# Kernel optimization log

Measured on AMD Instinct MI355X. Metric: run time of the kernel, lower is better.

## Reference

```python
import jax, jax.numpy as jnp
import numpy as np
from jax import lax

NUM_STEPS = 32
NUM_CLASSES = 10
HIDDEN = 1024


def setup_inputs() -> dict:
    key = jax.random.key(0)
    ks = jax.random.split(key, 4)
    B, H, W, C = 8, 1024, 2048, 4
    x = jax.random.normal(ks[0], (B, H, W, C), dtype=jnp.float32)
    conv_w = jax.random.normal(ks[1], (C,), dtype=jnp.float32) * 0.5
    conv_b = jnp.zeros((1,), dtype=jnp.float32)
    w1 = jax.random.normal(ks[2], (HIDDEN, W), dtype=jnp.float32) * (1.0 / np.sqrt(W))
    b1 = jnp.zeros((HIDDEN,), dtype=jnp.float32)
    w2 = jax.random.normal(ks[3], (NUM_CLASSES, HIDDEN), dtype=jnp.float32) * (1.0 / np.sqrt(HIDDEN))
    b2 = jnp.zeros((NUM_CLASSES,), dtype=jnp.float32)
    beta1 = jnp.full((1,), 0.95, dtype=jnp.float32)
    thr1 = jnp.ones((1,), dtype=jnp.float32)
    beta2 = jnp.full((1,), 0.95, dtype=jnp.float32)
    thr2 = jnp.ones((1,), dtype=jnp.float32)
    return {"x": x, "conv_w": conv_w, "conv_b": conv_b, "w1": w1, "b1": b1,
            "beta1": beta1, "thr1": thr1, "w2": w2, "b2": b2,
            "beta2": beta2, "thr2": thr2}


def _leaky_scan(inp_t, beta, thr):
    # inp_t: [T, ...]; snntorch Leaky, reset_mechanism='subtract', reset_delay=False
    b = jnp.clip(beta, 0.0, 1.0)

    def step(mem, u):
        mem = b * mem + u
        spk = (mem > thr).astype(u.dtype)   # heaviside spike
        mem = mem - spk * thr               # subtract reset (no delay)
        return mem, spk

    mem0 = jnp.zeros(inp_t.shape[1:], dtype=inp_t.dtype)
    _, spks = lax.scan(step, mem0, inp_t)
    return spks  # [T, ...]


def reference(x, conv_w, conv_b, w1, b1, beta1, thr1, w2, b2, beta2, thr2):
    # x: [B, H, W, 4]; 1x1 conv over 4 antenna channels -> 1 channel
    xf = jnp.einsum('bhwc,c->bhw', x, conv_w) + conv_b[0]       # [B, H, W]
    B, H, W = xf.shape
    G = H // NUM_STEPS
    xr = xf.reshape(B, G, NUM_STEPS, W)                          # [B, G, T, 2048]
    h = jnp.einsum('bgtw,dw->bgtd', xr, w1) + b1                 # [B, G, T, D]
    spks1 = _leaky_scan(jnp.moveaxis(h, 2, 0), beta1, thr1)      # [T, B, G, D]
    s = spks1.sum(axis=0)                                        # [B, G, D]
    h2 = jnp.einsum('bgd,cd->bgc', s, w2) + b2                   # [B, G, C]
    spks2 = _leaky_scan(jnp.moveaxis(h2, 1, 0), beta2, thr2)     # [G, B, C]
    logits = spks2.sum(axis=0)                                   # [B, C]
    return jax.nn.softmax(logits, axis=1)
```

## Files before the change

kernel.cpp:

```cpp
#include <hip/hip_runtime.h>

#define TSTEPS 32
#define HID 1024
#define NCLS 10
#define BATCH 8
#define GGRP 32
#define MROWS 8192
#define GK 2048
#define GN 1024
#define BUFSH 24576
#define CLDS 40

typedef __attribute__((ext_vector_type(8))) short bf16x8;
typedef __attribute__((ext_vector_type(16))) float f32x16;

__device__ __forceinline__ unsigned short bf16_rne(float v) {
    unsigned u = __builtin_bit_cast(unsigned, v);
    return (unsigned short)((u + 0x7FFFu + ((u >> 16) & 1u)) >> 16);
}
__device__ __forceinline__ float bf16_f(unsigned short h) {
    unsigned u = (unsigned)h << 16;
    return __builtin_bit_cast(float, u);
}
__device__ __forceinline__ void gload16(const unsigned short* g, unsigned short* l) {
    __builtin_amdgcn_global_load_lds(
        (const __attribute__((address_space(1))) void*)g,
        (__attribute__((address_space(3))) void*)l, 16, 0, 0);
}


__global__ __launch_bounds__(256) void conv_pack_kernel(
    const float4* __restrict__ x, const float* __restrict__ cw,
    const float* __restrict__ cb,
    unsigned short* __restrict__ Ahi, unsigned short* __restrict__ Alo)
{
    __shared__ __align__(16) unsigned short lh[128 * CLDS];
    __shared__ __align__(16) unsigned short ll[128 * CLDS];
    const int rb = blockIdx.x >> 6;
    const int kb = blockIdx.x & 63;
    const float c0 = cw[0], c1 = cw[1], c2 = cw[2], c3 = cw[3], cbv = cb[0];
    const int tid = threadIdx.x;

#pragma unroll
    for (int p = 0; p < 16; ++p) {
        int i = p * 256 + tid;
        int row = i >> 5, px = i & 31;
        float4 a = x[(size_t)(rb * 128 + row) * 2048 + kb * 32 + px];
        float v = a.x * c0 + a.y * c1 + a.z * c2 + a.w * c3 + cbv;
        unsigned short h = bf16_rne(v);
        lh[row * CLDS + px] = h;
        ll[row * CLDS + px] = bf16_rne(v - bf16_f(h));
    }
    __syncthreads();

#pragma unroll
    for (int cc = 0; cc < 2; ++cc) {
        int c = tid + cc * 256;
        int u = c >> 6, w = c & 63;
        int row = (u >> 1) * 32 + (w & 31);
        int ko  = (u & 1) * 2 + (w >> 5);
        bf16x8 h8 = *(const bf16x8*)(lh + row * CLDS + ko * 8);
        bf16x8 l8 = *(const bf16x8*)(ll + row * CLDS + ko * 8);
        size_t off = ((size_t)blockIdx.x * 512 + c) * 8;
        *(bf16x8*)(Ahi + off) = h8;
        *(bf16x8*)(Alo + off) = l8;
    }
}

__global__ __launch_bounds__(256) void wpack_kernel(
    const float* __restrict__ wsrc, unsigned short* __restrict__ Bhi,
    unsigned short* __restrict__ Blo)
{
    const int kb  = blockIdx.x & 63;
    const int cbk = blockIdx.x >> 6;
    const int tid = threadIdx.x;
#pragma unroll
    for (int cc = 0; cc < 4; ++cc) {
        int c = tid + cc * 256;
        int u = c >> 6, w = c & 63;
        int col = cbk * 256 + (u >> 1) * 32 + (w & 31);
        int k0  = kb * 32 + (u & 1) * 16 + (w >> 5) * 8;
        const float* pw = wsrc + ((size_t)col * 2048 + k0);
        bf16x8 h8, l8;
#pragma unroll
        for (int e = 0; e < 8; ++e) {
            float v = pw[e];
            unsigned short h = bf16_rne(v);
            h8[e] = (short)h;
            l8[e] = (short)bf16_rne(v - bf16_f(h));
        }
        size_t off = ((size_t)blockIdx.x * 1024 + c) * 8;
        *(bf16x8*)(Bhi + off) = h8;
        *(bf16x8*)(Blo + off) = l8;
    }
}

__global__ __launch_bounds__(512) void gemm_scan_kernel(
    const unsigned short* __restrict__ Ahi, const unsigned short* __restrict__ Alo,
    const unsigned short* __restrict__ Bhi, const unsigned short* __restrict__ Blo,
    const float* __restrict__ bias,
    const float* __restrict__ beta1, const float* __restrict__ thr1,
    float* __restrict__ S)
{
    __shared__ __align__(16) unsigned short sm[3 * BUFSH];

    const int tid = threadIdx.x;
    const int lane = tid & 63, wv = tid >> 6;
    const int wr = wv >> 2, wc = wv & 3;
    const int by = blockIdx.x & 63;
    const int bx = blockIdx.x >> 6;

    const unsigned short* gAh = Ahi + (size_t)by * 262144;
    const unsigned short* gAl = Alo + (size_t)by * 262144;
    const unsigned short* gBh = Bhi + (size_t)bx * 524288;
    const unsigned short* gBl = Blo + (size_t)bx * 524288;

    f32x16 acc[2][2];
#pragma unroll
    for (int i = 0; i < 2; ++i)
#pragma unroll
        for (int j = 0; j < 2; ++j) acc[i][j] = (f32x16)0.f;

    bf16x8 fr[2][16];

#define STAGE(buf, kb_)                                                          \
    {                                                                            \
        unsigned short* dst = sm + (buf) * BUFSH;                                \
        const size_t ao = (size_t)(kb_) * 4096 + tid * 8;                        \
        const size_t bo = (size_t)(kb_) * 8192 + tid * 8;                        \
        gload16(gAh + ao, dst + tid * 8);                                        \
        gload16(gAl + ao, dst + 4096 + tid * 8);                                 \
        gload16(gBh + bo, dst + 8192 + tid * 8);                                 \
        gload16(gBh + bo + 4096, dst + 12288 + tid * 8);                         \
        gload16(gBl + bo, dst + 16384 + tid * 8);                                \
        gload16(gBl + bo + 4096, dst + 20480 + tid * 8);                         \
    }

#define READF(s, bufp)                                                           \
    {                                                                            \
        const unsigned short* bp_ = (bufp);                                      \
        _Pragma("unroll")                                                        \
        for (int i = 0; i < 2; ++i)                                              \
            _Pragma("unroll")                                                    \
            for (int kh = 0; kh < 2; ++kh) {                                     \
                int ua = (((wr * 2 + i) * 2 + kh) << 9) + fo;                    \
                fr[s][(i * 2 + kh) * 2 + 0] = *(const bf16x8*)(bp_ + ua);        \
                fr[s][(i * 2 + kh) * 2 + 1] = *(const bf16x8*)(bp_ + 4096 + ua); \
            }                                                                    \
        _Pragma("unroll")                                                        \
        for (int j = 0; j < 2; ++j)                                              \
            _Pragma("unroll")                                                    \
            for (int kh = 0; kh < 2; ++kh) {                                     \
                int ub = (((wc * 2 + j) * 2 + kh) << 9) + fo;                    \
                fr[s][8 + (j * 2 + kh) * 2 + 0] = *(const bf16x8*)(bp_ + 8192 + ub);  \
                fr[s][8 + (j * 2 + kh) * 2 + 1] = *(const bf16x8*)(bp_ + 16384 + ub); \
            }                                                                    \
    }

#define MFMAF(s)                                                                 \
    {                                                                            \
        _Pragma("unroll")                                                        \
        for (int kh = 0; kh < 2; ++kh) {                                         \
            _Pragma("unroll")                                                    \
            for (int i = 0; i < 2; ++i)                                          \
                _Pragma("unroll")                                                \
                for (int j = 0; j < 2; ++j)                                      \
                    acc[i][j] = __builtin_amdgcn_mfma_f32_32x32x16_bf16(         \
                        fr[s][(i * 2 + kh) * 2], fr[s][8 + (j * 2 + kh) * 2],    \
                        acc[i][j], 0, 0, 0);                                     \
            _Pragma("unroll")                                                    \
            for (int i = 0; i < 2; ++i)                                          \
                _Pragma("unroll")                                                \
                for (int j = 0; j < 2; ++j)                                      \
                    acc[i][j] = __builtin_amdgcn_mfma_f32_32x32x16_bf16(         \
                        fr[s][(i * 2 + kh) * 2], fr[s][8 + (j * 2 + kh) * 2 + 1],\
                        acc[i][j], 0, 0, 0);                                     \
            _Pragma("unroll")                                                    \
            for (int i = 0; i < 2; ++i)                                          \
                _Pragma("unroll")                                                \
                for (int j = 0; j < 2; ++j)                                      \
                    acc[i][j] = __builtin_amdgcn_mfma_f32_32x32x16_bf16(         \
                        fr[s][(i * 2 + kh) * 2 + 1], fr[s][8 + (j * 2 + kh) * 2],\
                        acc[i][j], 0, 0, 0);                                     \
        }                                                                        \
    }

#define KSTEP(SC, SN, KB)                                                        \
    {                                                                            \
        if ((KB) < 63) asm volatile("s_waitcnt vmcnt(6)" ::: "memory");          \
        else           asm volatile("s_waitcnt vmcnt(0)" ::: "memory");          \
        asm volatile("s_waitcnt lgkmcnt(0)" ::: "memory");                       \
        __builtin_amdgcn_sched_barrier(0);                                       \
        __builtin_amdgcn_s_barrier();                                            \
        if ((KB) <= 61) STAGE(((KB) + 2) % 3, (KB) + 2);                         \
        READF(SN, sm + ((KB) % 3) * BUFSH);                                      \
        MFMAF(SC);                                                               \
    }

    STAGE(0, 0);
    STAGE(1, 1);
    STAGE(2, 2);
    asm volatile("s_waitcnt vmcnt(12)" ::: "memory");
    __builtin_amdgcn_s_barrier();
    const int fo = ((lane & 31) + 32 * (lane >> 5)) * 8;
    READF(0, sm);

    for (int kb = 1; kb < 63; kb += 2) {
        KSTEP(0, 1, kb);
        KSTEP(1, 0, kb + 1);
    }
    KSTEP(0, 1, 63);
    asm volatile("s_waitcnt lgkmcnt(0)" ::: "memory");
    __builtin_amdgcn_sched_barrier(0);
    MFMAF(1);
    __syncthreads();

    float* sb = (float*)sm;
    const float bclamp = fminf(fmaxf(beta1[0], 0.f), 1.f);
    const float th = thr1[0];
    const int sbg = tid >> 8;
    const int scol = tid & 255;
    const float bv = bias[bx * 256 + scol];

#pragma unroll
    for (int band = 0; band < 2; ++band) {
        if (wr == band) {
#pragma unroll
            for (int i = 0; i < 2; ++i)
#pragma unroll
                for (int j = 0; j < 2; ++j)
#pragma unroll
                    for (int r = 0; r < 16; ++r) {
                        int lr = i * 32 + (r & 3) + 8 * (r >> 2) + 4 * (lane >> 5);
                        int lc = wc * 64 + j * 32 + (lane & 31);
                        sb[lr * 256 + lc] = acc[i][j][r];
                    }
        }
        __syncthreads();
        float mem = 0.f, cnt = 0.f;
#pragma unroll
        for (int t = 0; t < TSTEPS; ++t) {
            float u = sb[(sbg * 32 + t) * 256 + scol] + bv;
            mem = bclamp * mem + u;
            float spk = mem > th ? 1.f : 0.f;
            mem -= spk * th;
            cnt += spk;
        }
        int bgg = by * 4 + band * 2 + sbg;
        S[(size_t)bgg * GN + bx * 256 + scol] = cnt;
        __syncthreads();
    }
}

__global__ __launch_bounds__(256) void fc2_kernel(
    const float* __restrict__ s, const float* __restrict__ w2,
    const float* __restrict__ b2, float* __restrict__ h2)
{
    int bg  = blockIdx.x;
    int tid = threadIdx.x;
    const float* sp = s + (size_t)bg * HID;
    float part[NCLS];
#pragma unroll
    for (int c = 0; c < NCLS; ++c) part[c] = 0.f;
    for (int d = tid; d < HID; d += 256) {
        float sv = sp[d];
#pragma unroll
        for (int c = 0; c < NCLS; ++c) part[c] += sv * w2[c * HID + d];
    }
#pragma unroll
    for (int c = 0; c < NCLS; ++c)
        for (int off = 32; off > 0; off >>= 1)
            part[c] += __shfl_down(part[c], off, 64);
    __shared__ float red[NCLS][4];
    int wave = tid >> 6, lanei = tid & 63;
    if (lanei == 0)
#pragma unroll
        for (int c = 0; c < NCLS; ++c) red[c][wave] = part[c];
    __syncthreads();
    if (tid < NCLS) {
        float v = red[tid][0] + red[tid][1] + red[tid][2] + red[tid][3] + b2[tid];
        h2[bg * NCLS + tid] = v;
    }
}

__global__ __launch_bounds__(128) void scan2_kernel(
    const float* __restrict__ h2, const float* __restrict__ beta2,
    const float* __restrict__ thr2, float* __restrict__ out)
{
    __shared__ float logits[BATCH][NCLS];
    int t = threadIdx.x;
    if (t < BATCH * NCLS) {
        int b = t / NCLS, c = t % NCLS;
        float bb = fminf(fmaxf(beta2[0], 0.f), 1.f);
        float th = thr2[0];
        float mem = 0.f, lg = 0.f;
        for (int g = 0; g < GGRP; ++g) {
            float u = h2[(b * GGRP + g) * NCLS + c];
            mem = bb * mem + u;
            float spk = mem > th ? 1.f : 0.f;
            mem -= spk * th;
            lg += spk;
        }
        logits[b][c] = lg;
    }
    __syncthreads();
    if (t < BATCH) {
        float mx = -1e30f;
        for (int c = 0; c < NCLS; ++c) mx = fmaxf(mx, logits[t][c]);
        float e[NCLS];
        float sum = 0.f;
        for (int c = 0; c < NCLS; ++c) { e[c] = expf(logits[t][c] - mx); sum += e[c]; }
        for (int c = 0; c < NCLS; ++c) out[t * NCLS + c] = e[c] / sum;
    }
}

extern "C" void kernel_launch(void* const* d_in, const int* in_sizes, int n_in,
                              void* d_out, int out_size, void* d_ws, size_t ws_size,
                              hipStream_t stream)
{
    const float* x     = (const float*)d_in[0];
    const float* cw    = (const float*)d_in[1];
    const float* cb    = (const float*)d_in[2];
    const float* w1    = (const float*)d_in[3];
    const float* b1    = (const float*)d_in[4];
    const float* beta1 = (const float*)d_in[5];
    const float* thr1  = (const float*)d_in[6];
    const float* w2    = (const float*)d_in[7];
    const float* b2    = (const float*)d_in[8];
    const float* beta2 = (const float*)d_in[9];
    const float* thr2  = (const float*)d_in[10];
    float* out = (float*)d_out;

    unsigned short* ahi = (unsigned short*)d_ws;
    unsigned short* alo = ahi + (size_t)MROWS * GK;
    unsigned short* bhi = alo + (size_t)MROWS * GK;
    unsigned short* blo = bhi + (size_t)GN * GK;
    float* s  = (float*)(blo + (size_t)GN * GK);
    float* h2 = s + (size_t)BATCH * GGRP * HID;

    conv_pack_kernel<<<4096, 256, 0, stream>>>((const float4*)x, cw, cb, ahi, alo);
    wpack_kernel    <<<256, 256, 0, stream>>>(w1, bhi, blo);
    gemm_scan_kernel<<<256, 512, 0, stream>>>(ahi, alo, bhi, blo, b1, beta1, thr1, s);
    fc2_kernel      <<<256, 256, 0, stream>>>(s, w2, b2, h2);
    scan2_kernel    <<<1, 128, 0, stream>>>(h2, beta2, thr2, out);
}
```

Before: 154.9 us.

## Split GEMM tiles to 128x128 with 256-thread blocks and double buffering

Halves the GEMM N-tile from 256 to 128 columns, so the grid doubles to 512 blocks of 256 threads (4 waves in a 2x2 layout). The B packing and the wpack grid change to match. The LDS pipeline drops from triple to double buffering, and each step now waits on vmcnt(0). The intent is better CU occupancy (two blocks per CU, 512 blocks over 256 CUs), at the cost of less load/compute overlap and twice the A-tile traffic. The spike scan epilogue is simplified to a single LDS pass.

```diff
diff --git a/kernel.cpp b/kernel.cpp
--- a/kernel.cpp
+++ b/kernel.cpp
@@ -8,7 +8,7 @@
 #define MROWS 8192
 #define GK 2048
 #define GN 1024
-#define BUFSH 24576
+#define BUFSH 16384
 #define CLDS 40
 
 typedef __attribute__((ext_vector_type(8))) short bf16x8;
@@ -75,12 +75,12 @@
     const int cbk = blockIdx.x >> 6;
     const int tid = threadIdx.x;
 #pragma unroll
-    for (int cc = 0; cc < 4; ++cc) {
+    for (int cc = 0; cc < 2; ++cc) {
         int c = tid + cc * 256;
         int u = c >> 6, w = c & 63;
-        int col = cbk * 256 + (u >> 1) * 32 + (w & 31);
-        int k0  = kb * 32 + (u & 1) * 16 + (w >> 5) * 8;
-        const float* pw = wsrc + ((size_t)col * 2048 + k0);
+        int row = (u >> 1) * 32 + (w & 31);
+        int k0  = (u & 1) * 16 + (w >> 5) * 8;
+        const float* pw = wsrc + ((size_t)(cbk * 128 + row) * 2048 + kb * 32 + k0);
         bf16x8 h8, l8;
 #pragma unroll
         for (int e = 0; e < 8; ++e) {
@@ -89,31 +89,31 @@
             h8[e] = (short)h;
             l8[e] = (short)bf16_rne(v - bf16_f(h));
         }
-        size_t off = ((size_t)blockIdx.x * 1024 + c) * 8;
+        size_t off = ((size_t)blockIdx.x * 512 + c) * 8;
         *(bf16x8*)(Bhi + off) = h8;
         *(bf16x8*)(Blo + off) = l8;
     }
 }
 
-__global__ __launch_bounds__(512) void gemm_scan_kernel(
+__global__ __launch_bounds__(256, 2) void gemm_scan_kernel(
     const unsigned short* __restrict__ Ahi, const unsigned short* __restrict__ Alo,
     const unsigned short* __restrict__ Bhi, const unsigned short* __restrict__ Blo,
     const float* __restrict__ bias,
     const float* __restrict__ beta1, const float* __restrict__ thr1,
     float* __restrict__ S)
 {
-    __shared__ __align__(16) unsigned short sm[3 * BUFSH];
+    __shared__ __align__(16) unsigned short sm[2 * BUFSH];
 
     const int tid = threadIdx.x;
     const int lane = tid & 63, wv = tid >> 6;
-    const int wr = wv >> 2, wc = wv & 3;
+    const int wr = wv >> 1, wc = wv & 1;
     const int by = blockIdx.x & 63;
     const int bx = blockIdx.x >> 6;
 
     const unsigned short* gAh = Ahi + (size_t)by * 262144;
     const unsigned short* gAl = Alo + (size_t)by * 262144;
-    const unsigned short* gBh = Bhi + (size_t)bx * 524288;
-    const unsigned short* gBl = Blo + (size_t)bx * 524288;
+    const unsigned short* gBh = Bhi + (size_t)bx * 262144;
+    const unsigned short* gBl = Blo + (size_t)bx * 262144;
 
     f32x16 acc[2][2];
 #pragma unroll
@@ -125,15 +125,16 @@
 
 #define STAGE(buf, kb_)                                                          \
     {                                                                            \
-        unsigned short* dst = sm + (buf) * BUFSH;                                \
-        const size_t ao = (size_t)(kb_) * 4096 + tid * 8;                        \
-        const size_t bo = (size_t)(kb_) * 8192 + tid * 8;                        \
-        gload16(gAh + ao, dst + tid * 8);                                        \
-        gload16(gAl + ao, dst + 4096 + tid * 8);                                 \
-        gload16(gBh + bo, dst + 8192 + tid * 8);                                 \
-        gload16(gBh + bo + 4096, dst + 12288 + tid * 8);                         \
-        gload16(gBl + bo, dst + 16384 + tid * 8);                                \
-        gload16(gBl + bo + 4096, dst + 20480 + tid * 8);                         \
+        unsigned short* dst = sm + (buf) * BUFSH + tid * 8;                      \
+        const size_t o = (size_t)(kb_) * 4096 + tid * 8;                         \
+        gload16(gAh + o, dst);                                                   \
+        gload16(gAh + o + 2048, dst + 2048);                                     \
+        gload16(gAl + o, dst + 4096);                                            \
+        gload16(gAl + o + 2048, dst + 6144);                                     \
+        gload16(gBh + o, dst + 8192);                                            \
+        gload16(gBh + o + 2048, dst + 10240);                                    \
+        gload16(gBl + o, dst + 12288);                                           \
+        gload16(gBl + o + 2048, dst + 14336);                                    \
     }
 
 #define READF(s, bufp)                                                           \
@@ -143,7 +144,7 @@
         for (int i = 0; i < 2; ++i)                                              \
             _Pragma("unroll")                                                    \
             for (int kh = 0; kh < 2; ++kh) {                                     \
-                int ua = (((wr * 2 + i) * 2 + kh) << 9) + fo;                    \
+                int ua = ((wr * 2 + i) * 2 + kh) * 512 + fo;                     \
                 fr[s][(i * 2 + kh) * 2 + 0] = *(const bf16x8*)(bp_ + ua);        \
                 fr[s][(i * 2 + kh) * 2 + 1] = *(const bf16x8*)(bp_ + 4096 + ua); \
             }                                                                    \
@@ -151,9 +152,9 @@
         for (int j = 0; j < 2; ++j)                                              \
             _Pragma("unroll")                                                    \
             for (int kh = 0; kh < 2; ++kh) {                                     \
-                int ub = (((wc * 2 + j) * 2 + kh) << 9) + fo;                    \
+                int ub = ((wc * 2 + j) * 2 + kh) * 512 + fo;                     \
                 fr[s][8 + (j * 2 + kh) * 2 + 0] = *(const bf16x8*)(bp_ + 8192 + ub);  \
-                fr[s][8 + (j * 2 + kh) * 2 + 1] = *(const bf16x8*)(bp_ + 16384 + ub); \
+                fr[s][8 + (j * 2 + kh) * 2 + 1] = *(const bf16x8*)(bp_ + 12288 + ub); \
             }                                                                    \
     }
 
@@ -185,31 +186,29 @@
         }                                                                        \
     }
 
-#define KSTEP(SC, SN, KB)                                                        \
+#define KSTEP(SC, SN, KB, DOSTAGE)                                               \
     {                                                                            \
-        if ((KB) < 63) asm volatile("s_waitcnt vmcnt(6)" ::: "memory");          \
-        else           asm volatile("s_waitcnt vmcnt(0)" ::: "memory");          \
+        asm volatile("s_waitcnt vmcnt(0)" ::: "memory");                         \
         asm volatile("s_waitcnt lgkmcnt(0)" ::: "memory");                       \
         __builtin_amdgcn_sched_barrier(0);                                       \
         __builtin_amdgcn_s_barrier();                                            \
-        if ((KB) <= 61) STAGE(((KB) + 2) % 3, (KB) + 2);                         \
-        READF(SN, sm + ((KB) % 3) * BUFSH);                                      \
+        if (DOSTAGE) STAGE(((KB) + 1) & 1, (KB) + 1);                            \
+        READF(SN, sm + ((KB) & 1) * BUFSH);                                      \
         MFMAF(SC);                                                               \
     }
 
     STAGE(0, 0);
     STAGE(1, 1);
-    STAGE(2, 2);
-    asm volatile("s_waitcnt vmcnt(12)" ::: "memory");
+    asm volatile("s_waitcnt vmcnt(8)" ::: "memory");
     __builtin_amdgcn_s_barrier();
     const int fo = ((lane & 31) + 32 * (lane >> 5)) * 8;
     READF(0, sm);
 
     for (int kb = 1; kb < 63; kb += 2) {
-        KSTEP(0, 1, kb);
-        KSTEP(1, 0, kb + 1);
-    }
-    KSTEP(0, 1, 63);
+        KSTEP(0, 1, kb, 1);
+        KSTEP(1, 0, kb + 1, 1);
+    }
+    KSTEP(0, 1, 63, 0);
     asm volatile("s_waitcnt lgkmcnt(0)" ::: "memory");
     __builtin_amdgcn_sched_barrier(0);
     MFMAF(1);
@@ -218,37 +217,35 @@
     float* sb = (float*)sm;
     const float bclamp = fminf(fmaxf(beta1[0], 0.f), 1.f);
     const float th = thr1[0];
-    const int sbg = tid >> 8;
-    const int scol = tid & 255;
-    const float bv = bias[bx * 256 + scol];
-
-#pragma unroll
-    for (int band = 0; band < 2; ++band) {
-        if (wr == band) {
-#pragma unroll
-            for (int i = 0; i < 2; ++i)
-#pragma unroll
-                for (int j = 0; j < 2; ++j)
-#pragma unroll
-                    for (int r = 0; r < 16; ++r) {
-                        int lr = i * 32 + (r & 3) + 8 * (r >> 2) + 4 * (lane >> 5);
-                        int lc = wc * 64 + j * 32 + (lane & 31);
-                        sb[lr * 256 + lc] = acc[i][j][r];
-                    }
-        }
-        __syncthreads();
+
+#pragma unroll
+    for (int i = 0; i < 2; ++i)
+#pragma unroll
+        for (int j = 0; j < 2; ++j)
+#pragma unroll
+            for (int r = 0; r < 16; ++r) {
+                int lr = wr * 64 + i * 32 + (r & 3) + 8 * (r >> 2) + 4 * (lane >> 5);
+                int lc = wc * 64 + j * 32 + (lane & 31);
+                sb[lr * 128 + lc] = acc[i][j][r];
+            }
+    __syncthreads();
+
+    const int scol = tid & 127;
+    const int half = tid >> 7;
+    const float bv = bias[bx * 128 + scol];
+#pragma unroll
+    for (int p = 0; p < 2; ++p) {
+        int gg = half * 2 + p;
         float mem = 0.f, cnt = 0.f;
 #pragma unroll
         for (int t = 0; t < TSTEPS; ++t) {
-            float u = sb[(sbg * 32 + t) * 256 + scol] + bv;
+            float u = sb[(gg * 32 + t) * 128 + scol] + bv;
             mem = bclamp * mem + u;
             float spk = mem > th ? 1.f : 0.f;
             mem -= spk * th;
             cnt += spk;
         }
-        int bgg = by * 4 + band * 2 + sbg;
-        S[(size_t)bgg * GN + bx * 256 + scol] = cnt;
-        __syncthreads();
+        S[(size_t)(by * 4 + gg) * GN + bx * 128 + scol] = cnt;
     }
 }
 
@@ -339,8 +336,8 @@
     float* h2 = s + (size_t)BATCH * GGRP * HID;
 
     conv_pack_kernel<<<4096, 256, 0, stream>>>((const float4*)x, cw, cb, ahi, alo);
-    wpack_kernel    <<<256, 256, 0, stream>>>(w1, bhi, blo);
-    gemm_scan_kernel<<<256, 512, 0, stream>>>(ahi, alo, bhi, blo, b1, beta1, thr1, s);
+    wpack_kernel    <<<512, 256, 0, stream>>>(w1, bhi, blo);
+    gemm_scan_kernel<<<512, 256, 0, stream>>>(ahi, alo, bhi, blo, b1, beta1, thr1, s);
     fc2_kernel      <<<256, 256, 0, stream>>>(s, w2, b2, h2);
     scan2_kernel    <<<1, 128, 0, stream>>>(h2, beta2, thr2, out);
 }
```

Measured after the change: 163.3 us. +5.5%, slower.

## Restructure GEMM main loop into half-K phases with split staging and setprio

Applied to the files above, without the earlier changes.

The K-loop is reorganised into two phases per K-block. Each phase reads only half the LDS fragments (8 instead of 16 registers), issues half of the next global-to-LDS stage, then runs 12 MFMAs between barriers. MFMA execution is wrapped in s_setprio so other waves' memory issue interleaves, which is meant to smooth load/compute overlap and cut register pressure. In exchange each K-block now carries extra barriers and loses the double-buffered fragment prefetch across steps.

```diff
diff --git a/kernel.cpp b/kernel.cpp
--- a/kernel.cpp
+++ b/kernel.cpp
@@ -121,98 +121,95 @@
 #pragma unroll
         for (int j = 0; j < 2; ++j) acc[i][j] = (f32x16)0.f;
 
-    bf16x8 fr[2][16];
-
-#define STAGE(buf, kb_)                                                          \
+    bf16x8 fr[8];
+    const int fo = ((lane & 31) + 32 * (lane >> 5)) * 8;
+
+#define STAGE_H(buf, kb_, half)                                                  \
     {                                                                            \
         unsigned short* dst = sm + (buf) * BUFSH;                                \
         const size_t ao = (size_t)(kb_) * 4096 + tid * 8;                        \
         const size_t bo = (size_t)(kb_) * 8192 + tid * 8;                        \
-        gload16(gAh + ao, dst + tid * 8);                                        \
-        gload16(gAl + ao, dst + 4096 + tid * 8);                                 \
-        gload16(gBh + bo, dst + 8192 + tid * 8);                                 \
-        gload16(gBh + bo + 4096, dst + 12288 + tid * 8);                         \
-        gload16(gBl + bo, dst + 16384 + tid * 8);                                \
-        gload16(gBl + bo + 4096, dst + 20480 + tid * 8);                         \
-    }
-
-#define READF(s, bufp)                                                           \
+        if ((half) == 0) {                                                       \
+            gload16(gAh + ao, dst + tid * 8);                                    \
+            gload16(gAl + ao, dst + 4096 + tid * 8);                             \
+            gload16(gBh + bo, dst + 8192 + tid * 8);                             \
+        } else {                                                                 \
+            gload16(gBh + bo + 4096, dst + 12288 + tid * 8);                     \
+            gload16(gBl + bo, dst + 16384 + tid * 8);                            \
+            gload16(gBl + bo + 4096, dst + 20480 + tid * 8);                     \
+        }                                                                        \
+    }
+
+#define MFMA12()                                                                 \
+    {                                                                            \
+        _Pragma("unroll")                                                        \
+        for (int i = 0; i < 2; ++i)                                              \
+            _Pragma("unroll")                                                    \
+            for (int j = 0; j < 2; ++j)                                          \
+                acc[i][j] = __builtin_amdgcn_mfma_f32_32x32x16_bf16(             \
+                    fr[i * 2 + 0], fr[4 + j * 2 + 0], acc[i][j], 0, 0, 0);       \
+        _Pragma("unroll")                                                        \
+        for (int i = 0; i < 2; ++i)                                              \
+            _Pragma("unroll")                                                    \
+            for (int j = 0; j < 2; ++j)                                          \
+                acc[i][j] = __builtin_amdgcn_mfma_f32_32x32x16_bf16(             \
+                    fr[i * 2 + 0], fr[4 + j * 2 + 1], acc[i][j], 0, 0, 0);       \
+        _Pragma("unroll")                                                        \
+        for (int i = 0; i < 2; ++i)                                              \
+            _Pragma("unroll")                                                    \
+            for (int j = 0; j < 2; ++j)                                          \
+                acc[i][j] = __builtin_amdgcn_mfma_f32_32x32x16_bf16(             \
+                    fr[i * 2 + 1], fr[4 + j * 2 + 0], acc[i][j], 0, 0, 0);       \
+    }
+
+#define PHASE(bufp, KH, DOSTAGE, SBUF, SKB, HALF, DOVM, VMC)                     \
     {                                                                            \
         const unsigned short* bp_ = (bufp);                                      \
         _Pragma("unroll")                                                        \
-        for (int i = 0; i < 2; ++i)                                              \
-            _Pragma("unroll")                                                    \
-            for (int kh = 0; kh < 2; ++kh) {                                     \
-                int ua = (((wr * 2 + i) * 2 + kh) << 9) + fo;                    \
-                fr[s][(i * 2 + kh) * 2 + 0] = *(const bf16x8*)(bp_ + ua);        \
-                fr[s][(i * 2 + kh) * 2 + 1] = *(const bf16x8*)(bp_ + 4096 + ua); \
-            }                                                                    \
-        _Pragma("unroll")                                                        \
-        for (int j = 0; j < 2; ++j)                                              \
-            _Pragma("unroll")                                                    \
-            for (int kh = 0; kh < 2; ++kh) {                                     \
-                int ub = (((wc * 2 + j) * 2 + kh) << 9) + fo;                    \
-                fr[s][8 + (j * 2 + kh) * 2 + 0] = *(const bf16x8*)(bp_ + 8192 + ub);  \
-                fr[s][8 + (j * 2 + kh) * 2 + 1] = *(const bf16x8*)(bp_ + 16384 + ub); \
-            }                                                                    \
-    }
-
-#define MFMAF(s)                                                                 \
-    {                                                                            \
-        _Pragma("unroll")                                                        \
-        for (int kh = 0; kh < 2; ++kh) {                                         \
-            _Pragma("unroll")                                                    \
-            for (int i = 0; i < 2; ++i)                                          \
-                _Pragma("unroll")                                                \
-                for (int j = 0; j < 2; ++j)                                      \
-                    acc[i][j] = __builtin_amdgcn_mfma_f32_32x32x16_bf16(         \
-                        fr[s][(i * 2 + kh) * 2], fr[s][8 + (j * 2 + kh) * 2],    \
-                        acc[i][j], 0, 0, 0);                                     \
-            _Pragma("unroll")                                                    \
-            for (int i = 0; i < 2; ++i)                                          \
-                _Pragma("unroll")                                                \
-                for (int j = 0; j < 2; ++j)                                      \
-                    acc[i][j] = __builtin_amdgcn_mfma_f32_32x32x16_bf16(         \
-                        fr[s][(i * 2 + kh) * 2], fr[s][8 + (j * 2 + kh) * 2 + 1],\
-                        acc[i][j], 0, 0, 0);                                     \
-            _Pragma("unroll")                                                    \
-            for (int i = 0; i < 2; ++i)                                          \
-                _Pragma("unroll")                                                \
-                for (int j = 0; j < 2; ++j)                                      \
-                    acc[i][j] = __builtin_amdgcn_mfma_f32_32x32x16_bf16(         \
-                        fr[s][(i * 2 + kh) * 2 + 1], fr[s][8 + (j * 2 + kh) * 2],\
-                        acc[i][j], 0, 0, 0);                                     \
+        for (int i = 0; i < 2; ++i) {                                            \
+            int ua = (((wr * 2 + i) * 2 + (KH)) << 9) + fo;                      \
+            fr[i * 2 + 0] = *(const bf16x8*)(bp_ + ua);                          \
+            fr[i * 2 + 1] = *(const bf16x8*)(bp_ + 4096 + ua);                   \
         }                                                                        \
-    }
-
-#define KSTEP(SC, SN, KB)                                                        \
-    {                                                                            \
-        if ((KB) < 63) asm volatile("s_waitcnt vmcnt(6)" ::: "memory");          \
-        else           asm volatile("s_waitcnt vmcnt(0)" ::: "memory");          \
+        _Pragma("unroll")                                                        \
+        for (int j = 0; j < 2; ++j) {                                            \
+            int ub = (((wc * 2 + j) * 2 + (KH)) << 9) + fo;                      \
+            fr[4 + j * 2 + 0] = *(const bf16x8*)(bp_ + 8192 + ub);               \
+            fr[4 + j * 2 + 1] = *(const bf16x8*)(bp_ + 16384 + ub);              \
+        }                                                                        \
+        if (DOSTAGE) STAGE_H(SBUF, SKB, HALF);                                   \
+        if (DOVM) asm volatile("s_waitcnt vmcnt(" #VMC ")" ::: "memory");        \
+        __builtin_amdgcn_s_barrier();                                            \
         asm volatile("s_waitcnt lgkmcnt(0)" ::: "memory");                       \
         __builtin_amdgcn_sched_barrier(0);                                       \
+        __builtin_amdgcn_s_setprio(1);                                           \
+        MFMA12();                                                                \
+        __builtin_amdgcn_s_setprio(0);                                           \
         __builtin_amdgcn_s_barrier();                                            \
-        if ((KB) <= 61) STAGE(((KB) + 2) % 3, (KB) + 2);                         \
-        READF(SN, sm + ((KB) % 3) * BUFSH);                                      \
-        MFMAF(SC);                                                               \
-    }
-
-    STAGE(0, 0);
-    STAGE(1, 1);
-    STAGE(2, 2);
+    }
+
+    STAGE_H(0, 0, 0); STAGE_H(0, 0, 1);
+    STAGE_H(1, 1, 0); STAGE_H(1, 1, 1);
+    STAGE_H(2, 2, 0); STAGE_H(2, 2, 1);
     asm volatile("s_waitcnt vmcnt(12)" ::: "memory");
     __builtin_amdgcn_s_barrier();
-    const int fo = ((lane & 31) + 32 * (lane >> 5)) * 8;
-    READF(0, sm);
-
-    for (int kb = 1; kb < 63; kb += 2) {
-        KSTEP(0, 1, kb);
-        KSTEP(1, 0, kb + 1);
-    }
-    KSTEP(0, 1, 63);
-    asm volatile("s_waitcnt lgkmcnt(0)" ::: "memory");
-    __builtin_amdgcn_sched_barrier(0);
-    MFMAF(1);
+
+    PHASE(sm, 0, 0, 0, 0, 0, 0, 0);
+    PHASE(sm, 1, 0, 0, 0, 0, 1, 6);
+
+    int cur = 1;
+    for (int kb = 1; kb <= 61; ++kb) {
+        const unsigned short* bp = sm + cur * BUFSH;
+        int stg = (cur == 0) ? 2 : cur - 1;
+        PHASE(bp, 0, 1, stg, kb + 2, 0, 0, 0);
+        PHASE(bp, 1, 1, stg, kb + 2, 1, 1, 6);
+        cur = (cur == 2) ? 0 : cur + 1;
+    }
+    PHASE(sm + 2 * BUFSH, 0, 0, 0, 0, 0, 0, 0);
+    PHASE(sm + 2 * BUFSH, 1, 0, 0, 0, 0, 1, 0);
+    PHASE(sm, 0, 0, 0, 0, 0, 0, 0);
+    PHASE(sm, 1, 0, 0, 0, 0, 0, 0);
+
     __syncthreads();
 
     float* sb = (float*)sm;
```

Result: slower. 159.7 us (+3.1%).

## Fuse antenna conv and bf16 split packing into the GEMM main loop

Applied to the files above, without the earlier changes.

Removes the separate conv_pack kernel and its intermediate bf16 hi/lo A buffers. The GEMM now loads raw fp32 x into registers two steps ahead, computes the 1x1 conv and hi/lo split in-kernel, and writes A tiles to a double-buffered LDS region while B stays triple-buffered via global_load_lds. This saves one launch and the A write/read round trip, but each x row band is now re-read by four column blocks in fp32, which raises global traffic. Register pressure also rises from the staged float4 arrays.

```diff
diff --git a/kernel.cpp b/kernel.cpp
--- a/kernel.cpp
+++ b/kernel.cpp
@@ -8,8 +8,6 @@
 #define MROWS 8192
 #define GK 2048
 #define GN 1024
-#define BUFSH 24576
-#define CLDS 40
 
 typedef __attribute__((ext_vector_type(8))) short bf16x8;
 typedef __attribute__((ext_vector_type(16))) float f32x16;
@@ -28,44 +26,6 @@
         (__attribute__((address_space(3))) void*)l, 16, 0, 0);
 }
 
-
-__global__ __launch_bounds__(256) void conv_pack_kernel(
-    const float4* __restrict__ x, const float* __restrict__ cw,
-    const float* __restrict__ cb,
-    unsigned short* __restrict__ Ahi, unsigned short* __restrict__ Alo)
-{
-    __shared__ __align__(16) unsigned short lh[128 * CLDS];
-    __shared__ __align__(16) unsigned short ll[128 * CLDS];
-    const int rb = blockIdx.x >> 6;
-    const int kb = blockIdx.x & 63;
-    const float c0 = cw[0], c1 = cw[1], c2 = cw[2], c3 = cw[3], cbv = cb[0];
-    const int tid = threadIdx.x;
-
-#pragma unroll
-    for (int p = 0; p < 16; ++p) {
-        int i = p * 256 + tid;
-        int row = i >> 5, px = i & 31;
-        float4 a = x[(size_t)(rb * 128 + row) * 2048 + kb * 32 + px];
-        float v = a.x * c0 + a.y * c1 + a.z * c2 + a.w * c3 + cbv;
-        unsigned short h = bf16_rne(v);
-        lh[row * CLDS + px] = h;
-        ll[row * CLDS + px] = bf16_rne(v - bf16_f(h));
-    }
-    __syncthreads();
-
-#pragma unroll
-    for (int cc = 0; cc < 2; ++cc) {
-        int c = tid + cc * 256;
-        int u = c >> 6, w = c & 63;
-        int row = (u >> 1) * 32 + (w & 31);
-        int ko  = (u & 1) * 2 + (w >> 5);
-        bf16x8 h8 = *(const bf16x8*)(lh + row * CLDS + ko * 8);
-        bf16x8 l8 = *(const bf16x8*)(ll + row * CLDS + ko * 8);
-        size_t off = ((size_t)blockIdx.x * 512 + c) * 8;
-        *(bf16x8*)(Ahi + off) = h8;
-        *(bf16x8*)(Alo + off) = l8;
-    }
-}
 
 __global__ __launch_bounds__(256) void wpack_kernel(
     const float* __restrict__ wsrc, unsigned short* __restrict__ Bhi,
@@ -95,14 +55,15 @@
     }
 }
 
-__global__ __launch_bounds__(512) void gemm_scan_kernel(
-    const unsigned short* __restrict__ Ahi, const unsigned short* __restrict__ Alo,
+__global__ __launch_bounds__(512) void gemm_fused_kernel(
+    const float4* __restrict__ x,
     const unsigned short* __restrict__ Bhi, const unsigned short* __restrict__ Blo,
+    const float* __restrict__ cw, const float* __restrict__ cb,
     const float* __restrict__ bias,
     const float* __restrict__ beta1, const float* __restrict__ thr1,
     float* __restrict__ S)
 {
-    __shared__ __align__(16) unsigned short sm[3 * BUFSH];
+    __shared__ __align__(16) unsigned short sm[65536];
 
     const int tid = threadIdx.x;
     const int lane = tid & 63, wv = tid >> 6;
@@ -110,8 +71,13 @@
     const int by = blockIdx.x & 63;
     const int bx = blockIdx.x >> 6;
 
-    const unsigned short* gAh = Ahi + (size_t)by * 262144;
-    const unsigned short* gAl = Alo + (size_t)by * 262144;
+    const float c0 = cw[0], c1 = cw[1], c2 = cw[2], c3 = cw[3], cbv = cb[0];
+
+    const int cu_ = tid >> 6, cww = tid & 63;
+    const int arow = (cu_ >> 1) * 32 + (cww & 31);
+    const int ak0  = (cu_ & 1) * 16 + (cww >> 5) * 8;
+    const float4* px = x + (size_t)(by * 128 + arow) * 2048 + ak0;
+
     const unsigned short* gBh = Bhi + (size_t)bx * 524288;
     const unsigned short* gBl = Blo + (size_t)bx * 524288;
 
@@ -121,43 +87,66 @@
 #pragma unroll
         for (int j = 0; j < 2; ++j) acc[i][j] = (f32x16)0.f;
 
-    bf16x8 fr[2][16];
-
-#define STAGE(buf, kb_)                                                          \
-    {                                                                            \
-        unsigned short* dst = sm + (buf) * BUFSH;                                \
-        const size_t ao = (size_t)(kb_) * 4096 + tid * 8;                        \
-        const size_t bo = (size_t)(kb_) * 8192 + tid * 8;                        \
-        gload16(gAh + ao, dst + tid * 8);                                        \
-        gload16(gAl + ao, dst + 4096 + tid * 8);                                 \
-        gload16(gBh + bo, dst + 8192 + tid * 8);                                 \
-        gload16(gBh + bo + 4096, dst + 12288 + tid * 8);                         \
-        gload16(gBl + bo, dst + 16384 + tid * 8);                                \
-        gload16(gBl + bo + 4096, dst + 20480 + tid * 8);                         \
-    }
-
-#define READF(s, bufp)                                                           \
-    {                                                                            \
-        const unsigned short* bp_ = (bufp);                                      \
+    bf16x8 fr[16];
+    float4 xs0[8], xs1[8];
+    const int fo = ((lane & 31) + 32 * (lane >> 5)) * 8;
+
+#define LOADX(XS, KB_)                                                           \
+    {                                                                            \
+        const float4* p_ = px + (size_t)(KB_) * 32;                              \
+        _Pragma("unroll")                                                        \
+        for (int e = 0; e < 8; ++e) XS[e] = p_[e];                               \
+    }
+
+#define CONVW(XS, KB_)                                                           \
+    {                                                                            \
+        bf16x8 h8, l8;                                                           \
+        _Pragma("unroll")                                                        \
+        for (int e = 0; e < 8; ++e) {                                            \
+            float4 a = XS[e];                                                    \
+            float v = a.x * c0 + a.y * c1 + a.z * c2 + a.w * c3 + cbv;           \
+            unsigned short h = bf16_rne(v);                                      \
+            h8[e] = (short)h;                                                    \
+            l8[e] = (short)bf16_rne(v - bf16_f(h));                              \
+        }                                                                        \
+        unsigned short* d_ = sm + ((KB_) & 1) * 8192 + tid * 8;                  \
+        *(bf16x8*)d_ = h8;                                                       \
+        *(bf16x8*)(d_ + 4096) = l8;                                              \
+    }
+
+#define STAGE_B(KB_)                                                             \
+    {                                                                            \
+        unsigned short* dst = sm + 16384 + ((KB_) % 3) * 16384;                  \
+        const size_t bo = (size_t)(KB_) * 8192 + tid * 8;                        \
+        gload16(gBh + bo, dst + tid * 8);                                        \
+        gload16(gBh + bo + 4096, dst + 4096 + tid * 8);                          \
+        gload16(gBl + bo, dst + 8192 + tid * 8);                                 \
+        gload16(gBl + bo + 4096, dst + 12288 + tid * 8);                         \
+    }
+
+#define READF(KB_)                                                               \
+    {                                                                            \
+        const unsigned short* ab = sm + ((KB_) & 1) * 8192;                      \
+        const unsigned short* bb = sm + 16384 + ((KB_) % 3) * 16384;             \
         _Pragma("unroll")                                                        \
         for (int i = 0; i < 2; ++i)                                              \
             _Pragma("unroll")                                                    \
             for (int kh = 0; kh < 2; ++kh) {                                     \
                 int ua = (((wr * 2 + i) * 2 + kh) << 9) + fo;                    \
-                fr[s][(i * 2 + kh) * 2 + 0] = *(const bf16x8*)(bp_ + ua);        \
-                fr[s][(i * 2 + kh) * 2 + 1] = *(const bf16x8*)(bp_ + 4096 + ua); \
+                fr[(i * 2 + kh) * 2 + 0] = *(const bf16x8*)(ab + ua);            \
+                fr[(i * 2 + kh) * 2 + 1] = *(const bf16x8*)(ab + 4096 + ua);     \
             }                                                                    \
         _Pragma("unroll")                                                        \
         for (int j = 0; j < 2; ++j)                                              \
             _Pragma("unroll")                                                    \
             for (int kh = 0; kh < 2; ++kh) {                                     \
                 int ub = (((wc * 2 + j) * 2 + kh) << 9) + fo;                    \
-                fr[s][8 + (j * 2 + kh) * 2 + 0] = *(const bf16x8*)(bp_ + 8192 + ub);  \
-                fr[s][8 + (j * 2 + kh) * 2 + 1] = *(const bf16x8*)(bp_ + 16384 + ub); \
+                fr[8 + (j * 2 + kh) * 2 + 0] = *(const bf16x8*)(bb + ub);        \
+                fr[8 + (j * 2 + kh) * 2 + 1] = *(const bf16x8*)(bb + 8192 + ub); \
             }                                                                    \
     }
 
-#define MFMAF(s)                                                                 \
+#define MFMAF()                                                                  \
     {                                                                            \
         _Pragma("unroll")                                                        \
         for (int kh = 0; kh < 2; ++kh) {                                         \
@@ -166,53 +155,68 @@
                 _Pragma("unroll")                                                \
                 for (int j = 0; j < 2; ++j)                                      \
                     acc[i][j] = __builtin_amdgcn_mfma_f32_32x32x16_bf16(         \
-                        fr[s][(i * 2 + kh) * 2], fr[s][8 + (j * 2 + kh) * 2],    \
+                        fr[(i * 2 + kh) * 2], fr[8 + (j * 2 + kh) * 2],          \
                         acc[i][j], 0, 0, 0);                                     \
             _Pragma("unroll")                                                    \
             for (int i = 0; i < 2; ++i)                                          \
                 _Pragma("unroll")                                                \
                 for (int j = 0; j < 2; ++j)                                      \
                     acc[i][j] = __builtin_amdgcn_mfma_f32_32x32x16_bf16(         \
-                        fr[s][(i * 2 + kh) * 2], fr[s][8 + (j * 2 + kh) * 2 + 1],\
+                        fr[(i * 2 + kh) * 2], fr[8 + (j * 2 + kh) * 2 + 1],      \
                         acc[i][j], 0, 0, 0);                                     \
             _Pragma("unroll")                                                    \
             for (int i = 0; i < 2; ++i)                                          \
                 _Pragma("unroll")                                                \
                 for (int j = 0; j < 2; ++j)                                      \
                     acc[i][j] = __builtin_amdgcn_mfma_f32_32x32x16_bf16(         \
-                        fr[s][(i * 2 + kh) * 2 + 1], fr[s][8 + (j * 2 + kh) * 2],\
+                        fr[(i * 2 + kh) * 2 + 1], fr[8 + (j * 2 + kh) * 2],      \
                         acc[i][j], 0, 0, 0);                                     \
         }                                                                        \
     }
 
-#define KSTEP(SC, SN, KB)                                                        \
-    {                                                                            \
-        if ((KB) < 63) asm volatile("s_waitcnt vmcnt(6)" ::: "memory");          \
-        else           asm volatile("s_waitcnt vmcnt(0)" ::: "memory");          \
+#define ITER(XC, XL, KB, DOSTAGE, DOLOAD, DOCONV)                                \
+    {                                                                            \
         asm volatile("s_waitcnt lgkmcnt(0)" ::: "memory");                       \
         __builtin_amdgcn_sched_barrier(0);                                       \
         __builtin_amdgcn_s_barrier();                                            \
-        if ((KB) <= 61) STAGE(((KB) + 2) % 3, (KB) + 2);                         \
-        READF(SN, sm + ((KB) % 3) * BUFSH);                                      \
-        MFMAF(SC);                                                               \
-    }
-
-    STAGE(0, 0);
-    STAGE(1, 1);
-    STAGE(2, 2);
-    asm volatile("s_waitcnt vmcnt(12)" ::: "memory");
+        READF(KB);                                                               \
+        if (DOCONV) CONVW(XC, (KB) + 1);                                         \
+        if (DOSTAGE) STAGE_B((KB) + 2);                                          \
+        __builtin_amdgcn_sched_barrier(0);       \
+        if (DOLOAD) LOADX(XL, (KB) + 2);                                         \
+        asm volatile("s_waitcnt lgkmcnt(0)" ::: "memory");                       \
+        __builtin_amdgcn_sched_barrier(0);                                       \
+        __builtin_amdgcn_s_setprio(1);                                           \
+        MFMAF();                                                                 \
+        __builtin_amdgcn_s_setprio(0);                                           \
+    }
+
+    STAGE_B(0);
+    __builtin_amdgcn_sched_barrier(0);
+    LOADX(xs0, 0);
+    __builtin_amdgcn_sched_barrier(0);
+    STAGE_B(1);
+    __builtin_amdgcn_sched_barrier(0);
+    LOADX(xs1, 1);
+    CONVW(xs0, 0);
+    asm volatile("s_waitcnt lgkmcnt(0)" ::: "memory");
+    __builtin_amdgcn_sched_barrier(0);
     __builtin_amdgcn_s_barrier();
-    const int fo = ((lane & 31) + 32 * (lane >> 5)) * 8;
-    READF(0, sm);
-
-    for (int kb = 1; kb < 63; kb += 2) {
-        KSTEP(0, 1, kb);
-        KSTEP(1, 0, kb + 1);
-    }
-    KSTEP(0, 1, 63);
+
+    ITER(xs1, xs0, 0, 1, 1, 1);
+    for (int kb = 1; kb < 61; kb += 2) {
+        ITER(xs0, xs1, kb, 1, 1, 1);
+        ITER(xs1, xs0, kb + 1, 1, 1, 1);
+    }
+    ITER(xs0, xs1, 61, 1, 1, 1);
+    ITER(xs1, xs0, 62, 0, 0, 1);
     asm volatile("s_waitcnt lgkmcnt(0)" ::: "memory");
     __builtin_amdgcn_sched_barrier(0);
-    MFMAF(1);
+    __builtin_amdgcn_s_barrier();
+    READF(63);
+    asm volatile("s_waitcnt lgkmcnt(0)" ::: "memory");
+    __builtin_amdgcn_sched_barrier(0);
+    MFMAF();
     __syncthreads();
 
     float* sb = (float*)sm;
@@ -331,16 +335,14 @@
     const float* thr2  = (const float*)d_in[10];
     float* out = (float*)d_out;
 
-    unsigned short* ahi = (unsigned short*)d_ws;
-    unsigned short* alo = ahi + (size_t)MROWS * GK;
-    unsigned short* bhi = alo + (size_t)MROWS * GK;
+    unsigned short* bhi = (unsigned short*)d_ws;
     unsigned short* blo = bhi + (size_t)GN * GK;
     float* s  = (float*)(blo + (size_t)GN * GK);
     float* h2 = s + (size_t)BATCH * GGRP * HID;
 
-    conv_pack_kernel<<<4096, 256, 0, stream>>>((const float4*)x, cw, cb, ahi, alo);
-    wpack_kernel    <<<256, 256, 0, stream>>>(w1, bhi, blo);
-    gemm_scan_kernel<<<256, 512, 0, stream>>>(ahi, alo, bhi, blo, b1, beta1, thr1, s);
-    fc2_kernel      <<<256, 256, 0, stream>>>(s, w2, b2, h2);
-    scan2_kernel    <<<1, 128, 0, stream>>>(h2, beta2, thr2, out);
-}
+    wpack_kernel     <<<256, 256, 0, stream>>>(w1, bhi, blo);
+    gemm_fused_kernel<<<256, 512, 0, stream>>>((const float4*)x, bhi, blo, cw, cb,
+                                               b1, beta1, thr1, s);
+    fc2_kernel       <<<256, 256, 0, stream>>>(s, w2, b2, h2);
+    scan2_kernel     <<<1, 128, 0, stream>>>(h2, beta2, thr2, out);
+}
```

After: 209.3 us. 1.35x slower.
